# Optimization experiments

Measured on AMD Instinct MI355X. Metric: run time of the kernel, lower is better.

The kernel has to match this reference:

```python
import jax, jax.numpy as jnp
import numpy as np

B = 1024        # query batch
M = 16384       # memory_size
D = 256         # feature_dim
A = (D // 8 + 1) * 8   # attention_dim = 264
H = 8           # num heads
DH = A // H     # head dim = 33


def setup_inputs() -> dict:
    key = jax.random.key(0)
    ks = jax.random.split(key, 16)
    s = 0.02
    return {
        "features": jax.random.normal(ks[0], (B, D), jnp.float32),
        "gradients": jax.random.normal(ks[1], (B, D), jnp.float32),
        "memory_keys": jax.random.normal(ks[2], (M, D), jnp.float32),
        "memory_values": jax.random.normal(ks[3], (M, D), jnp.float32),
        # feature_projector: Linear(D, A)
        "Wf": jax.random.normal(ks[4], (A, D), jnp.float32) * s,
        "bf": jnp.zeros((A,), jnp.float32),
        # MultiheadAttention in_proj (q, k, v), each Linear(A, A)
        "Wq": jax.random.normal(ks[5], (A, A), jnp.float32) * s,
        "Wk": jax.random.normal(ks[6], (A, A), jnp.float32) * s,
        "Wv": jax.random.normal(ks[7], (A, A), jnp.float32) * s,
        "bq": jnp.zeros((A,), jnp.float32),
        "bk": jnp.zeros((A,), jnp.float32),
        "bv": jnp.zeros((A,), jnp.float32),
        # MHA out_proj: Linear(A, A)
        "Wo": jax.random.normal(ks[8], (A, A), jnp.float32) * s,
        "bo": jnp.zeros((A,), jnp.float32),
        # output_projector: Linear(A, D)
        "Wout": jax.random.normal(ks[9], (D, A), jnp.float32) * s,
        "bout": jnp.zeros((D,), jnp.float32),
    }


def _forward(features, gradients, memory_keys, memory_values,
             Wf, bf, Wq, Wk, Wv, bq, bk, bv, Wo, bo, Wout, bout):
    # ---- compute_surprise: grad norm * min cdist(features, memory_keys) ----
    grad_mag = jnp.linalg.norm(gradients, axis=-1)                 # [B]
    f2 = jnp.sum(features * features, axis=-1, keepdims=True)      # [B,1]
    m2 = jnp.sum(memory_keys * memory_keys, axis=-1)               # [M]
    d2 = f2 + m2[None, :] - 2.0 * (features @ memory_keys.T)       # [B,M]
    dist = jnp.sqrt(jnp.maximum(d2, 0.0))
    min_dist = jnp.min(dist, axis=-1)                              # [B]
    surprise = grad_mag * min_dist                                 # [B]

    # ---- read_memory: project, MHA (q_len=1), output projection ----
    q = features @ Wf.T + bf          # [B,A]
    k = memory_keys @ Wf.T + bf       # [M,A]
    v = memory_values @ Wf.T + bf     # [M,A]

    qh = (q @ Wq.T + bq).reshape(B, H, DH)   # [B,H,DH]
    kh = (k @ Wk.T + bk).reshape(M, H, DH)   # [M,H,DH]
    vh = (v @ Wv.T + bv).reshape(M, H, DH)   # [M,H,DH]

    scale = 1.0 / jnp.sqrt(jnp.asarray(DH, qh.dtype))
    scores = jnp.einsum('bhd,mhd->bhm', qh, kh) * scale            # [B,H,M]
    attn = jax.nn.softmax(scores, axis=-1)
    ctx = jnp.einsum('bhm,mhd->bhd', attn, vh).reshape(B, A)       # [B,A]
    attn_out = ctx @ Wo.T + bo                                     # [B,A]
    retrieved = attn_out @ Wout.T + bout                           # [B,D]
    return retrieved, surprise


def reference(features, gradients, memory_keys, memory_values,
              Wf, bf, Wq, Wk, Wv, bq, bk, bv, Wo, bo, Wout, bout):
    return _forward(features, gradients, memory_keys, memory_values,
                    Wf, bf, Wq, Wk, Wv, bq, bk, bv, Wo, bo, Wout, bout)
```

## Files before the change

kernel.cpp:

```cpp
#include <hip/hip_runtime.h>
#include <math.h>

#define B_Q 1024
#define MEM 16384
#define DF  256
#define AD  264
#define NH  8
#define SPLIT 16
#define SCALE 0.17407765595569785f

typedef __attribute__((ext_vector_type(8)))  short bf16x8;
typedef __attribute__((ext_vector_type(4)))  float f32x4;
typedef __attribute__((ext_vector_type(16))) float f32x16;
typedef __attribute__((ext_vector_type(8)))  unsigned short u16x8;
typedef __attribute__((ext_vector_type(4)))  unsigned short u16x4;
typedef __fp16 fp16x2 __attribute__((ext_vector_type(2)));
typedef _Float16 f16x8 __attribute__((ext_vector_type(8)));

#define MFMA16(a,b,c)  __builtin_amdgcn_mfma_f32_16x16x32_bf16((a),(b),(c),0,0,0)
#define MFMA32(a,b,c)  __builtin_amdgcn_mfma_f32_32x32x16_bf16((a),(b),(c),0,0,0)
#define MFMA32H(a,b,c) __builtin_amdgcn_mfma_f32_32x32x16_f16((a),(b),(c),0,0,0)

__device__ __forceinline__ unsigned short f2bf(float x) {
  unsigned int u = __float_as_uint(x);
  return (unsigned short)((u + 0x7fffu + ((u >> 16) & 1u)) >> 16);
}
union uhw { fp16x2 h; unsigned u; };
__device__ __forceinline__ unsigned short f2h(float x) {
  uhw t; t.h = __builtin_amdgcn_cvt_pkrtz(x, x);
  return (unsigned short)(t.u & 0xFFFFu);
}
__device__ __forceinline__ unsigned pk_fma_f16(unsigned a, unsigned b, unsigned c) {
  unsigned d;
  asm("v_pk_fma_f16 %0, %1, %2, %3" : "=v"(d) : "v"(a), "v"(b), "v"(c));
  return d;
}
__device__ __forceinline__ void plswap(unsigned &x, unsigned &y) {
  asm volatile("v_permlane32_swap_b32 %0, %1" : "+v"(x), "+v"(y));
}
__device__ __forceinline__ void gload_lds16(const void* g, void* l) {
  __builtin_amdgcn_global_load_lds(
      (const __attribute__((address_space(1))) unsigned int*)g,
      (__attribute__((address_space(3))) unsigned int*)l, 16, 0, 0);
}

__global__ __launch_bounds__(256) void prelude_kernel(
    const float* __restrict__ f, const float* __restrict__ g,
    const float* __restrict__ k, const float* __restrict__ v,
    const float* __restrict__ Wq, const float* __restrict__ Wk,
    const float* __restrict__ Wv, const float* __restrict__ Wout,
    const float* __restrict__ Wf, const float* __restrict__ Wo,
    unsigned short* __restrict__ Fbf, unsigned short* __restrict__ Kbf,
    unsigned short* __restrict__ Vbf,
    float* __restrict__ f2, float* __restrict__ g2, float* __restrict__ m2,
    unsigned short* __restrict__ out6, float4* __restrict__ zreg)
{
  const int bid = blockIdx.x, t = threadIdx.x;
  if (bid < 4352) {
    zreg[bid*256 + t] = float4{0.f, 0.f, 0.f, 0.f};
  } else if (bid < 13056) {
    int gid = (bid - 4352) * 256 + t;
    int w = gid >> 6, lane = gid & 63;
    const float* src; unsigned short* dst; float* nrm; int row;
    if (w < 1024)       { row = w;         src = f + (size_t)row*DF; dst = Fbf + (size_t)row*DF; nrm = f2 + row; }
    else if (w < 2048)  { row = w - 1024;  src = g + (size_t)row*DF; dst = 0;                    nrm = g2 + row; }
    else if (w < 18432) { row = w - 2048;  src = k + (size_t)row*DF; dst = Kbf + (size_t)row*DF; nrm = m2 + row; }
    else                { row = w - 18432; src = v + (size_t)row*DF; dst = Vbf + (size_t)row*DF; nrm = 0; }
    float4 x = ((const float4*)src)[lane];
    if (dst) {
      u16x4 o; o[0]=f2bf(x.x); o[1]=f2bf(x.y); o[2]=f2bf(x.z); o[3]=f2bf(x.w);
      *(u16x4*)(dst + lane*4) = o;
    }
    if (nrm) {
      float s = x.x*x.x + x.y*x.y + x.z*x.z + x.w*x.w;
      #pragma unroll
      for (int off = 1; off < 64; off <<= 1) s += __shfl_xor(s, off, 64);
      if (lane == 0) *nrm = s;
    }
  } else {
    int gid = (bid - 13056) * 256 + t;
    if (gid >= 6*320*72) return;
    int arr = gid / (320*72);
    int rem = gid - arr*(320*72);
    int a = rem / 72;
    int c4 = (rem - a*72) * 4;
    u16x4 pk;
    #pragma unroll
    for (int i = 0; i < 4; ++i) {
      int c = c4 + i;
      float vv = 0.f;
      if (c < AD) {
        if (arr < 3)      { const float* s = arr==0?Wq:arr==1?Wk:Wv; if (a < AD) vv = s[a*AD + c]; }
        else if (arr == 3){ if (a < DF) vv = Wout[a*AD + c]; }
        else if (arr == 4){ if (a < DF) vv = Wf[c*DF + a]; }
        else              { if (a < AD) vv = Wo[c*AD + a]; }
      }
      pk[i] = f2bf(vv);
    }
    *(u16x4*)(out6 + (size_t)gid * 4) = pk;
  }
}

__global__ __launch_bounds__(256) void combine_kernel(
    const unsigned short* __restrict__ W6,
    const float* __restrict__ Wq, const float* __restrict__ Wk,
    const float* __restrict__ Wv, const float* __restrict__ Wout,
    const float* __restrict__ bf, const float* __restrict__ bq,
    const float* __restrict__ bk, const float* __restrict__ bv,
    const float* __restrict__ bo, const float* __restrict__ bout,
    unsigned short* __restrict__ WfQbf, unsigned short* __restrict__ WfKbf,
    unsigned short* __restrict__ WfVbf, unsigned short* __restrict__ Wco_b,
    float* __restrict__ bqp, float* __restrict__ bkp,
    float* __restrict__ bvp, float* __restrict__ bco)
{
  const float QS = SCALE * 1.4426950408889634f;
  const int bid = blockIdx.x;
  if (bid < 80) {
    const int seg = bid / 20, sub = bid % 20;
    int bm, bn; const unsigned short *X, *Wt;
    if (seg < 3) { bm = (sub >> 2)*64; bn = (sub & 3)*64;
                   X = W6 + (size_t)seg*320*288; Wt = W6 + (size_t)4*320*288; }
    else         { bm = (sub / 5)*64; bn = (sub % 5)*64;
                   X = W6 + (size_t)3*320*288; Wt = W6 + (size_t)5*320*288; }
    const int t = threadIdx.x, wid = t >> 6, lane = t & 63;
    const int lq = lane & 15, lg = lane >> 4;
    const int r0 = bm + wid*16;
    bf16x8 af[9];
    const unsigned short* arow = X + (size_t)(r0 + lq) * 288;
    #pragma unroll
    for (int c = 0; c < 9; ++c) af[c] = *(const bf16x8*)(arow + c*32 + lg*8);
    f32x4 acc[4] = {};
    #pragma unroll
    for (int c = 0; c < 9; ++c) {
      #pragma unroll
      for (int tt = 0; tt < 4; ++tt) {
        const unsigned short* brow = Wt + (size_t)(bn + tt*16 + lq) * 288;
        bf16x8 bw = *(const bf16x8*)(brow + c*32 + lg*8);
        acc[tt] = MFMA16(af[c], bw, acc[tt]);
      }
    }
    if (seg < 3) {
      unsigned short* Od = (seg == 0) ? WfQbf : (seg == 1) ? WfKbf : WfVbf;
      float sc = (seg == 0) ? QS : 1.0f;
      #pragma unroll
      for (int tt = 0; tt < 4; ++tt) {
        int col = bn + tt*16 + lq;
        #pragma unroll
        for (int j = 0; j < 4; ++j) {
          int row = r0 + lg*4 + j;
          if (row < AD) Od[row*256 + col] = f2bf(acc[tt][j] * sc);
        }
      }
    } else {
      #pragma unroll
      for (int tt = 0; tt < 4; ++tt) {
        int col = bn + tt*16 + lq;
        #pragma unroll
        for (int j = 0; j < 4; ++j) {
          int row = r0 + lg*4 + j;
          if (col < 288) Wco_b[row*288 + col] = (col < AD) ? f2bf(acc[tt][j]) : (unsigned short)0;
        }
      }
    }
  } else {
    int gw = (bid - 80) * 4 + (threadIdx.x >> 6);
    int lane = threadIdx.x & 63;
    const float* Wsrc; const float* vin; const float* badd; float* dst;
    int row; float sc = 1.0f;
    if (gw < 264)      { Wsrc = Wq;   vin = bf; badd = bq;   dst = bqp; row = gw;       sc = QS; }
    else if (gw < 528) { Wsrc = Wk;   vin = bf; badd = bk;   dst = bkp; row = gw - 264; }
    else if (gw < 792) { Wsrc = Wv;   vin = bf; badd = bv;   dst = bvp; row = gw - 528; }
    else               { Wsrc = Wout; vin = bo; badd = bout; dst = bco; row = gw - 792; }
    float s = 0.f;
    for (int c = lane; c < AD; c += 64) s = fmaf(Wsrc[row*AD + c], vin[c], s);
    #pragma unroll
    for (int off = 1; off < 64; off <<= 1) s += __shfl_xor(s, off, 64);
    if (lane == 0) dst[row] = (badd[row] + s) * sc;
  }
}

__global__ __launch_bounds__(256) void proj3_kernel(
    const unsigned short* __restrict__ Fbf, const unsigned short* __restrict__ Kbf,
    const unsigned short* __restrict__ Vbf,
    const unsigned short* __restrict__ WfQbf, const unsigned short* __restrict__ WfKbf,
    const unsigned short* __restrict__ WfVbf,
    const float* __restrict__ bqp, const float* __restrict__ bkp,
    const float* __restrict__ bvp,
    unsigned short* __restrict__ qh, unsigned short* __restrict__ kh,
    unsigned short* __restrict__ vhT)
{
  __shared__ unsigned short Wl[64*256];
  const int bid = blockIdx.x;
  const unsigned short *X, *W; const float* bias; unsigned short* out;
  int bx, by, R, transposed;
  if (bid < 40)       { X = Fbf; W = WfQbf; bias = bqp; out = qh;  R = B_Q; transposed = 0;
                        bx = bid % 8;           by = bid / 8; }
  else if (bid < 680) { X = Kbf; W = WfKbf; bias = bkp; out = kh;  R = MEM; transposed = 0;
                        bx = (bid - 40) % 128;  by = (bid - 40) / 128; }
  else                { X = Vbf; W = WfVbf; bias = bvp; out = vhT; R = MEM; transposed = 1;
                        bx = (bid - 680) % 128; by = (bid - 680) / 128; }
  const int t = threadIdx.x, wid = t >> 6, lane = t & 63;
  const int lq = lane & 15, lg = lane >> 4;
  const int a0 = by * 64;

  {
    const char* Bb = (const char*)W;
    int rowl = (lane >> 3);
    int cb  = (lane & 7) * 16;
    #pragma unroll
    for (int s = 0; s < 8; ++s) {
      int r = s*8 + rowl;
      gload_lds16(Bb + (size_t)(a0 + r)*512 + wid*128 + (cb ^ ((r & 7) << 4)),
                  (char*)Wl + (wid*8 + s)*1024);
    }
  }
  const int ar0 = bx * 128 + wid * 32;
  const unsigned short* arow0 = X + (size_t)(ar0 + lq) * 256 + lg*8;
  const unsigned short* arow1 = arow0 + 16*256;
  __syncthreads();

  f32x4 acc[2][4] = {};
  #pragma unroll
  for (int c = 0; c < 8; ++c) {
    bf16x8 a0f = *(const bf16x8*)(arow0 + c*32);
    bf16x8 a1f = *(const bf16x8*)(arow1 + c*32);
    #pragma unroll
    for (int tt = 0; tt < 4; ++tt) {
      int rb = tt*16 + lq;
      bf16x8 bw = *(const bf16x8*)((const char*)Wl + (c >> 1)*8192 + rb*128
                                   + (((c & 1)*64 + lg*16) ^ ((rb & 7) << 4)));
      acc[0][tt] = MFMA16(a0f, bw, acc[0][tt]);
      acc[1][tt] = MFMA16(a1f, bw, acc[1][tt]);
    }
  }
  #pragma unroll
  for (int tt = 0; tt < 4; ++tt) {
    int a = a0 + tt*16 + lq;
    if (a < AD) {
      int h = a / 33;
      int dh = a - h * 33;
      float bv = bias[a];
      #pragma unroll
      for (int i = 0; i < 2; ++i) {
        if (!transposed) {
          #pragma unroll
          for (int j = 0; j < 4; ++j) {
            int row = ar0 + i*16 + lg*4 + j;
            out[((size_t)h * R + row) * 64 + dh] = f2bf(acc[i][tt][j] + bv);
          }
        } else {
          u16x4 pk;
          #pragma unroll
          for (int j = 0; j < 4; ++j) pk[j] = f2h(acc[i][tt][j] + bv);
          *(u16x4*)(out + ((size_t)h * 48 + dh) * (size_t)MEM + ar0 + i*16 + lg*4) = pk;
        }
      }
    }
  }
}

__global__ __launch_bounds__(512) void fused_sa_kernel(
    const unsigned short* __restrict__ Fbf, const unsigned short* __restrict__ Kbf,
    const float* __restrict__ f2, const float* __restrict__ m2,
    float* __restrict__ pmin,
    const unsigned short* __restrict__ qh, const unsigned short* __restrict__ kh,
    const unsigned short* __restrict__ vhT,
    float* __restrict__ part_l, float* __restrict__ part_ctx)
{
  __shared__ unsigned short smem[64*256];
  const int id = blockIdx.x;
  const int t = threadIdx.x, wid = t >> 6, lane = t & 63;
  const int lq = lane & 15, lg = lane >> 4;

  if (id < 1024) {
    unsigned short* Bt = smem;
    const int bm = (id >> 8) * 256;
    const int bn = id & 255;
    const int bc = bn * 64;
    {
      const char* Bb = (const char*)Kbf;
      const int kchunk = wid >> 1, half = wid & 1;
      int rowl = (lane >> 3);
      int cb  = (lane & 7) * 16;
      #pragma unroll
      for (int s = 0; s < 4; ++s) {
        int r = half*32 + s*8 + rowl;
        gload_lds16(Bb + (size_t)(bc + r)*512 + kchunk*128 + (cb ^ ((r & 7) << 4)),
                    (char*)Bt + (kchunk*8 + half*4 + s)*1024);
      }
    }
    const int ar0 = bm + wid*32;
    const unsigned short* arow0 = Fbf + (size_t)(ar0 + lq) * 256 + lg*8;
    const unsigned short* arow1 = arow0 + 16*256;
    __syncthreads();
    f32x4 acc[2][4] = {};
    #pragma unroll
    for (int c = 0; c < 8; ++c) {
      bf16x8 a0 = *(const bf16x8*)(arow0 + c*32);
      bf16x8 a1 = *(const bf16x8*)(arow1 + c*32);
      #pragma unroll
      for (int tt = 0; tt < 4; ++tt) {
        int rb = tt*16 + lq;
        bf16x8 bw = *(const bf16x8*)((const char*)Bt + (c >> 1)*8192 + rb*128
                                     + (((c & 1)*64 + lg*16) ^ ((rb & 7) << 4)));
        acc[0][tt] = MFMA16(a0, bw, acc[0][tt]);
        acc[1][tt] = MFMA16(a1, bw, acc[1][tt]);
      }
    }
    #pragma unroll
    for (int i = 0; i < 2; ++i) {
      float rmin[4] = {1e30f, 1e30f, 1e30f, 1e30f};
      #pragma unroll
      for (int tt = 0; tt < 4; ++tt) {
        float m2c = m2[bc + tt*16 + lq];
        #pragma unroll
        for (int r = 0; r < 4; ++r) {
          float d2 = fmaxf(f2[ar0 + i*16 + lg*4 + r] + m2c - 2.0f*acc[i][tt][r], 0.f);
          rmin[r] = fminf(rmin[r], d2);
        }
      }
      #pragma unroll
      for (int off = 1; off < 16; off <<= 1)
        #pragma unroll
        for (int r = 0; r < 4; ++r) rmin[r] = fminf(rmin[r], __shfl_xor(rmin[r], off, 64));
      if (lq == 0) {
        #pragma unroll
        for (int r = 0; r < 4; ++r)
          pmin[(size_t)(ar0 + i*16 + lg*4 + r)*256 + bn] = rmin[r];
      }
    }
    return;
  }

  const int fid = id - 1024;
  const int l31 = lane & 31, lg2 = lane >> 5;
  const int qt = fid >> 7;
  const int pr = fid & 127;
  const int h = pr >> 4, sp = pr & 15;
  const int b0 = qt * 256;
  const int q  = b0 + wid*32 + l31;

  if (t < 64) {
    int bb = t >> 5;
    ((unsigned*)((char*)smem + 16384 + bb*8192 + 33*128))[t & 31] = 0x3C003C00u;
  }

  const unsigned c2u = 0x33B133B1u;
  const unsigned c1u = 0x398C398Cu;
  const unsigned oneu = 0x3C003C00u;
  auto p2 = [&](float a, float b) -> unsigned {
    uhw x; x.h = __builtin_amdgcn_cvt_pkrtz(a, b);
    unsigned tq = pk_fma_f16(x.u, c2u, c1u);
    return pk_fma_f16(x.u, tq, oneu);
  };

  bf16x8 qA[3];
  {
    const unsigned short* qrow = qh + ((size_t)h * B_Q + q) * 64;
    #pragma unroll
    for (int c = 0; c < 3; ++c) qA[c] = *(const bf16x8*)(qrow + c*16 + lg2*8);
  }

  f32x16 ctx0 = {}, ctx1 = {};
  const char* khb = (const char*)kh + (size_t)h * MEM * 128;
  const char* vhb = (const char*)vhT + (size_t)h * 48 * MEM * 2;
  const int m00 = sp * 1024;

  auto stageA = [&](int bb, int m0) {
    {
      int row = wid*8 + (lane >> 3);
      int cb  = (lane & 7) * 16;
      gload_lds16(khb + (size_t)(m0 + row)*128 + (cb ^ ((row & 7) << 4)),
                  (char*)smem + bb*8192 + wid*1024);
    }
    if (wid < 5) {
      int d  = wid*8 + (lane >> 3);
      int cb = (lane & 7) * 16;
      if (d <= 32)
        gload_lds16(vhb + ((size_t)d * MEM + m0)*2 + (cb ^ ((d & 7) << 4)),
                    (char*)smem + 16384 + bb*8192 + wid*1024);
    }
  };

  stageA(0, m00);
  for (int it = 0; it < 16; ++it) {
    const int cur = it & 1;
    __syncthreads();
    if (it < 15) stageA(cur ^ 1, m00 + (it + 1) * 64);
    const char* ktb = (const char*)smem + cur*8192;
    const char* vtb = (const char*)smem + 16384 + cur*8192;
    #pragma unroll
    for (int ms = 0; ms < 2; ++ms) {
      f32x16 s16 = {};
      {
        const char* krow = ktb + (ms*32 + l31)*128;
        __builtin_amdgcn_s_setprio(1);
        #pragma unroll
        for (int c = 0; c < 3; ++c) {
          bf16x8 kb = *(const bf16x8*)(krow + ((c*32 + lg2*16) ^ ((l31 & 7) << 4)));
          s16 = MFMA32(kb, qA[c], s16);
        }
        __builtin_amdgcn_s_setprio(0);
      }
      unsigned w0a = p2(s16[0],  s16[1]);
      unsigned w1a = p2(s16[2],  s16[3]);
      unsigned w2a = p2(s16[4],  s16[5]);
      unsigned w3a = p2(s16[6],  s16[7]);
      unsigned w0b = p2(s16[8],  s16[9]);
      unsigned w1b = p2(s16[10], s16[11]);
      unsigned w2b = p2(s16[12], s16[13]);
      unsigned w3b = p2(s16[14], s16[15]);
      plswap(w0a, w2a); plswap(w1a, w3a);
      plswap(w0b, w2b); plswap(w1b, w3b);
      union { unsigned u[4]; f16x8 v; } paA, paB;
      paA.u[0]=w0a; paA.u[1]=w1a; paA.u[2]=w2a; paA.u[3]=w3a;
      paB.u[0]=w0b; paB.u[1]=w1b; paB.u[2]=w2b; paB.u[3]=w3b;
      const int swd = ((l31 & 7) << 4);
      {
        int cb = ms*64;
        f16x8 v0 = *(const f16x8*)(vtb + l31*128      + ((cb + lg2*16) ^ swd));
        f16x8 v1 = *(const f16x8*)(vtb + (32+l31)*128 + ((cb + lg2*16) ^ swd));
        f16x8 v2 = *(const f16x8*)(vtb + l31*128      + ((cb + 32 + lg2*16) ^ swd));
        f16x8 v3 = *(const f16x8*)(vtb + (32+l31)*128 + ((cb + 32 + lg2*16) ^ swd));
        __builtin_amdgcn_s_setprio(1);
        ctx0 = MFMA32H(paA.v, v0, ctx0);
        ctx1 = MFMA32H(paA.v, v1, ctx1);
        ctx0 = MFMA32H(paB.v, v2, ctx0);
        ctx1 = MFMA32H(paB.v, v3, ctx1);
        __builtin_amdgcn_s_setprio(0);
      }
    }
  }
  #pragma unroll
  for (int r = 0; r < 16; ++r) {
    int ql = (r & 3) + 8*(r >> 2) + 4*lg2;
    int b  = b0 + wid*32 + ql;
    size_t pidx = (((size_t)b * NH) + h) * SPLIT + sp;
    part_ctx[pidx*33 + l31] = ctx0[r];
    if (l31 == 0) part_ctx[pidx*33 + 32] = ctx1[r];
    if (l31 == 1) part_l[pidx] = ctx1[r];
  }
}

__global__ __launch_bounds__(256) void combine2_kernel(
    const float* __restrict__ pl, const float* __restrict__ pc,
    unsigned short* __restrict__ ctxb,
    const float* __restrict__ pmin, const float* __restrict__ g2,
    float* __restrict__ out)
{
  const int bid = blockIdx.x;
  if (bid < 2048) {
    int w    = (bid * 256 + threadIdx.x) >> 6;
    int lane = threadIdx.x & 63;
    int b = w >> 3, h = w & 7;
    size_t base = (size_t)w * SPLIT;
    float L = 0.f;
    #pragma unroll
    for (int s = 0; s < SPLIT; ++s) L += pl[base+s];
    if (lane < 33) {
      float cv = 0.f;
      #pragma unroll
      for (int s = 0; s < SPLIT; ++s) cv += pc[(base+s)*33 + lane];
      ctxb[(size_t)b*288 + h*33 + lane] = f2bf(cv / L);
    } else if (h == 7 && lane < 57) {
      ctxb[(size_t)b*288 + 231 + lane] = 0;
    }
  } else {
    int row  = (bid - 2048) * 4 + (threadIdx.x >> 6);
    int lane = threadIdx.x & 63;
    float4 v = ((const float4*)(pmin + (size_t)row*256))[lane];
    float m = fminf(fminf(v.x, v.y), fminf(v.z, v.w));
    #pragma unroll
    for (int off = 1; off < 64; off <<= 1) m = fminf(m, __shfl_xor(m, off, 64));
    if (lane == 0)
      out[(size_t)B_Q * DF + row] = sqrtf(g2[row]) * sqrtf(fmaxf(m, 0.f));
  }
}

__global__ __launch_bounds__(256) void out_mfma_kernel(
    const unsigned short* __restrict__ ctxb, const unsigned short* __restrict__ Wco_b,
    const float* __restrict__ bco, float* __restrict__ out)
{
  const int t = threadIdx.x, wid = t >> 6, lane = t & 63;
  const int lq = lane & 15, lg = lane >> 4;
  const int r0 = blockIdx.x * 64 + wid * 16;
  const int d0 = blockIdx.y * 64;
  bf16x8 af[9];
  const unsigned short* arow = ctxb + (size_t)(r0 + lq) * 288;
  #pragma unroll
  for (int c = 0; c < 9; ++c) af[c] = *(const bf16x8*)(arow + c*32 + lg*8);
  f32x4 acc[4] = {};
  #pragma unroll
  for (int c = 0; c < 9; ++c) {
    #pragma unroll
    for (int tt = 0; tt < 4; ++tt) {
      const unsigned short* brow = Wco_b + (size_t)(d0 + tt*16 + lq) * 288;
      bf16x8 bw = *(const bf16x8*)(brow + c*32 + lg*8);
      acc[tt] = MFMA16(af[c], bw, acc[tt]);
    }
  }
  #pragma unroll
  for (int tt = 0; tt < 4; ++tt) {
    int d = d0 + tt*16 + lq;
    float bv = bco[d];
    #pragma unroll
    for (int j = 0; j < 4; ++j)
      out[(size_t)(r0 + lg*4 + j) * 256 + d] = acc[tt][j] + bv;
  }
}

extern "C" void kernel_launch(void* const* d_in, const int* in_sizes, int n_in,
                              void* d_out, int out_size, void* d_ws, size_t ws_size,
                              hipStream_t stream)
{
  const float* features  = (const float*)d_in[0];
  const float* gradients = (const float*)d_in[1];
  const float* keys      = (const float*)d_in[2];
  const float* values    = (const float*)d_in[3];
  const float* Wf   = (const float*)d_in[4];
  const float* bf   = (const float*)d_in[5];
  const float* Wq   = (const float*)d_in[6];
  const float* Wk   = (const float*)d_in[7];
  const float* Wv   = (const float*)d_in[8];
  const float* bq   = (const float*)d_in[9];
  const float* bk   = (const float*)d_in[10];
  const float* bv   = (const float*)d_in[11];
  const float* Wo   = (const float*)d_in[12];
  const float* bo   = (const float*)d_in[13];
  const float* Wout = (const float*)d_in[14];
  const float* bout = (const float*)d_in[15];
  float* out = (float*)d_out;
  (void)ws_size; (void)n_in; (void)in_sizes; (void)out_size;

  char* Wp = (char*)d_ws;
  size_t o = 0;
  auto alloc = [&](size_t bytes) -> void* {
    void* p = Wp + o; o = (o + bytes + 255) & ~(size_t)255; return p;
  };
  unsigned short* W6   = (unsigned short*)alloc((size_t)6*320*288*2);
  unsigned short* Wco_b= (unsigned short*)alloc((size_t)256*288*2);
  unsigned short* ctxb = (unsigned short*)alloc((size_t)B_Q*288*2);
  float* bqp   = (float*)alloc(320*4);
  float* bkp   = (float*)alloc(320*4);
  float* bvp   = (float*)alloc(320*4);
  float* bco   = (float*)alloc(320*4);
  float* f2    = (float*)alloc(B_Q*4);
  float* g2    = (float*)alloc(B_Q*4);
  float* m2    = (float*)alloc(MEM*4);
  float* pmin  = (float*)alloc((size_t)B_Q*256*4);
  float* part_l = (float*)alloc((size_t)B_Q*NH*SPLIT*4);
  float* part_ctx = (float*)alloc((size_t)B_Q*NH*SPLIT*33*4);
  unsigned short* Fbf = (unsigned short*)alloc((size_t)B_Q*DF*2);
  unsigned short* Kbf = (unsigned short*)alloc((size_t)MEM*DF*2);
  unsigned short* Vbf = (unsigned short*)alloc((size_t)MEM*DF*2);
  unsigned short* WfQbf = (unsigned short*)alloc((size_t)320*256*2);
  unsigned short* WfKbf = (unsigned short*)alloc((size_t)320*256*2);
  unsigned short* WfVbf = (unsigned short*)alloc((size_t)320*256*2);
  unsigned short* qh  = (unsigned short*)alloc((size_t)NH*B_Q*64*2);
  unsigned short* kh  = (unsigned short*)alloc((size_t)NH*MEM*64*2);
  unsigned short* vhT = (unsigned short*)alloc((size_t)NH*48*MEM*2);

  prelude_kernel<<<13596, 256, 0, stream>>>(
      features, gradients, keys, values, Wq, Wk, Wv, Wout, Wf, Wo,
      Fbf, Kbf, Vbf, f2, g2, m2, W6, (float4*)qh);
  combine_kernel<<<342, 256, 0, stream>>>(
      W6, Wq, Wk, Wv, Wout, bf, bq, bk, bv, bo, bout,
      WfQbf, WfKbf, WfVbf, Wco_b, bqp, bkp, bvp, bco);
  proj3_kernel<<<1320, 256, 0, stream>>>(
      Fbf, Kbf, Vbf, WfQbf, WfKbf, WfVbf, bqp, bkp, bvp, qh, kh, vhT);
  fused_sa_kernel<<<1536, 512, 0, stream>>>(
      Fbf, Kbf, f2, m2, pmin, qh, kh, vhT, part_l, part_ctx);
  combine2_kernel<<<2304, 256, 0, stream>>>(part_l, part_ctx, ctxb, pmin, g2, out);
  out_mfma_kernel<<<dim3(B_Q/64, DF/64), 256, 0, stream>>>(ctxb, Wco_b, bco, out);
}
```

Before: 107.1 us.

## Load K tiles directly into registers instead of staging through LDS

K rows for the score MFMA are now read from global memory straight into registers, double-buffered as two register sets, while only the V tile is still staged in LDS. This halves LDS traffic and footprint and removes the LDS read of K, in exchange for higher register pressure and uncoalesced-ish per-lane global reads of K. The loop is manually unrolled by two to alternate register buffers, and the last iteration issues a redundant prefetch of tile 0.

```diff
diff --git a/kernel.cpp b/kernel.cpp
--- a/kernel.cpp
+++ b/kernel.cpp
@@ -342,7 +342,7 @@
 
   if (t < 64) {
     int bb = t >> 5;
-    ((unsigned*)((char*)smem + 16384 + bb*8192 + 33*128))[t & 31] = 0x3C003C00u;
+    ((unsigned*)((char*)smem + bb*8192 + 33*128))[t & 31] = 0x3C003C00u;
   }
 
   const unsigned c2u = 0x33B133B1u;
@@ -362,46 +362,35 @@
   }
 
   f32x16 ctx0 = {}, ctx1 = {};
-  const char* khb = (const char*)kh + (size_t)h * MEM * 128;
+  const unsigned short* khp = kh + (size_t)h * MEM * 64 + lg2*8;
   const char* vhb = (const char*)vhT + (size_t)h * 48 * MEM * 2;
   const int m00 = sp * 1024;
 
-  auto stageA = [&](int bb, int m0) {
-    {
-      int row = wid*8 + (lane >> 3);
-      int cb  = (lane & 7) * 16;
-      gload_lds16(khb + (size_t)(m0 + row)*128 + (cb ^ ((row & 7) << 4)),
-                  (char*)smem + bb*8192 + wid*1024);
-    }
+  auto stageV = [&](int bb, int m0) {
     if (wid < 5) {
       int d  = wid*8 + (lane >> 3);
       int cb = (lane & 7) * 16;
       if (d <= 32)
         gload_lds16(vhb + ((size_t)d * MEM + m0)*2 + (cb ^ ((d & 7) << 4)),
-                    (char*)smem + 16384 + bb*8192 + wid*1024);
+                    (char*)smem + bb*8192 + wid*1024);
     }
   };
-
-  stageA(0, m00);
-  for (int it = 0; it < 16; ++it) {
-    const int cur = it & 1;
-    __syncthreads();
-    if (it < 15) stageA(cur ^ 1, m00 + (it + 1) * 64);
-    const char* ktb = (const char*)smem + cur*8192;
-    const char* vtb = (const char*)smem + 16384 + cur*8192;
+  auto loadK = [&](bf16x8 (&kr)[2][3], int m0) {
+    #pragma unroll
+    for (int ms = 0; ms < 2; ++ms) {
+      const unsigned short* krow = khp + (size_t)(m0 + ms*32 + l31) * 64;
+      #pragma unroll
+      for (int c = 0; c < 3; ++c) kr[ms][c] = *(const bf16x8*)(krow + c*16);
+    }
+  };
+  auto computeTile = [&](const bf16x8 (&kr)[2][3], const char* vtb) {
     #pragma unroll
     for (int ms = 0; ms < 2; ++ms) {
       f32x16 s16 = {};
-      {
-        const char* krow = ktb + (ms*32 + l31)*128;
-        __builtin_amdgcn_s_setprio(1);
-        #pragma unroll
-        for (int c = 0; c < 3; ++c) {
-          bf16x8 kb = *(const bf16x8*)(krow + ((c*32 + lg2*16) ^ ((l31 & 7) << 4)));
-          s16 = MFMA32(kb, qA[c], s16);
-        }
-        __builtin_amdgcn_s_setprio(0);
-      }
+      __builtin_amdgcn_s_setprio(1);
+      #pragma unroll
+      for (int c = 0; c < 3; ++c) s16 = MFMA32(kr[ms][c], qA[c], s16);
+      __builtin_amdgcn_s_setprio(0);
       unsigned w0a = p2(s16[0],  s16[1]);
       unsigned w1a = p2(s16[2],  s16[3]);
       unsigned w2a = p2(s16[4],  s16[5]);
@@ -416,20 +405,37 @@
       paA.u[0]=w0a; paA.u[1]=w1a; paA.u[2]=w2a; paA.u[3]=w3a;
       paB.u[0]=w0b; paB.u[1]=w1b; paB.u[2]=w2b; paB.u[3]=w3b;
       const int swd = ((l31 & 7) << 4);
-      {
-        int cb = ms*64;
-        f16x8 v0 = *(const f16x8*)(vtb + l31*128      + ((cb + lg2*16) ^ swd));
-        f16x8 v1 = *(const f16x8*)(vtb + (32+l31)*128 + ((cb + lg2*16) ^ swd));
-        f16x8 v2 = *(const f16x8*)(vtb + l31*128      + ((cb + 32 + lg2*16) ^ swd));
-        f16x8 v3 = *(const f16x8*)(vtb + (32+l31)*128 + ((cb + 32 + lg2*16) ^ swd));
-        __builtin_amdgcn_s_setprio(1);
-        ctx0 = MFMA32H(paA.v, v0, ctx0);
-        ctx1 = MFMA32H(paA.v, v1, ctx1);
-        ctx0 = MFMA32H(paB.v, v2, ctx0);
-        ctx1 = MFMA32H(paB.v, v3, ctx1);
-        __builtin_amdgcn_s_setprio(0);
-      }
-    }
+      int cb = ms*64;
+      f16x8 v0 = *(const f16x8*)(vtb + l31*128      + ((cb + lg2*16) ^ swd));
+      f16x8 v1 = *(const f16x8*)(vtb + (32+l31)*128 + ((cb + lg2*16) ^ swd));
+      f16x8 v2 = *(const f16x8*)(vtb + l31*128      + ((cb + 32 + lg2*16) ^ swd));
+      f16x8 v3 = *(const f16x8*)(vtb + (32+l31)*128 + ((cb + 32 + lg2*16) ^ swd));
+      __builtin_amdgcn_s_setprio(1);
+      ctx0 = MFMA32H(paA.v, v0, ctx0);
+      ctx1 = MFMA32H(paA.v, v1, ctx1);
+      ctx0 = MFMA32H(paB.v, v2, ctx0);
+      ctx1 = MFMA32H(paB.v, v3, ctx1);
+      __builtin_amdgcn_s_setprio(0);
+    }
+  };
+
+  bf16x8 krA[2][3], krB[2][3];
+  loadK(krA, m00);
+  stageV(0, m00);
+  #pragma unroll 1
+  for (int it2 = 0; it2 < 8; ++it2) {
+    const int tA = 2*it2;
+    __syncthreads();
+    stageV(1, m00 + (tA + 1) * 64);
+    loadK(krB, m00 + (tA + 1) * 64);
+    computeTile(krA, (const char*)smem);
+    __syncthreads();
+    {
+      int nx = (tA + 2 < 16) ? tA + 2 : 0;
+      stageV(0, m00 + nx * 64);
+      loadK(krA, m00 + nx * 64);
+    }
+    computeTile(krB, (const char*)smem + 8192);
   }
   #pragma unroll
   for (int r = 0; r < 16; ++r) {
```

Measured after the change: 143.2 us. 1.34x slower.
